# Kernel tuning notes

Hardware: AMD Instinct MI355X
Metric: run time of the kernel (lower is better)

## Reference

```python
import jax, jax.numpy as jnp
import numpy as np

B, Q, K, DQ, DK, H, DV = 4, 1024, 1024, 256, 256, 64, 256

def setup_inputs() -> dict:
    key = jax.random.key(0)
    k1, k2, k3, k4, k5, k6 = jax.random.split(key, 6)
    queries = jax.random.normal(k1, (B, Q, DQ), dtype=jnp.float32)
    keys = jax.random.normal(k2, (B, K, DK), dtype=jnp.float32)
    values = jax.random.normal(k3, (B, K, DV), dtype=jnp.float32)
    # learned params (stored as (in, out) so x @ W matches nn.Linear)
    W_q = jax.random.normal(k4, (DQ, H), dtype=jnp.float32) / np.sqrt(DQ)
    W_k = jax.random.normal(k5, (DK, H), dtype=jnp.float32) / np.sqrt(DK)
    w_v = jax.random.normal(k6, (H,), dtype=jnp.float32) / np.sqrt(H)
    return {"queries": queries, "keys": keys, "values": values,
            "W_q": W_q, "W_k": W_k, "w_v": w_v}

def reference(queries, keys, values, W_q, W_k, w_v):
    # projections: [B,Q,H], [B,K,H]
    q = jnp.einsum('bqd,dh->bqh', queries, W_q)
    k = jnp.einsum('bkd,dh->bkh', keys, W_k)
    # broadcast add -> tanh -> reduce with w_v: scores [B,Q,K]
    features = jnp.tanh(q[:, :, None, :] + k[:, None, :, :])  # [B,Q,K,H]
    scores = jnp.einsum('bqkh,h->bqk', features, w_v)
    attn = jax.nn.softmax(scores, axis=-1)  # dropout is identity in eval
    return jnp.einsum('bqk,bkv->bqv', attn, values)
```

## Files before the change

kernel.cpp:

```cpp
#include <hip/hip_runtime.h>

#define Bn 4
#define Qn 1024
#define Kn 1024
#define Dd 256
#define Hh 64
#define Dv 256
#define TQ 16

typedef __attribute__((ext_vector_type(8))) short short8;
typedef __attribute__((ext_vector_type(4))) float floatx4;
typedef __attribute__((ext_vector_type(2))) float floatx2;

__device__ __forceinline__ floatx2 fma2(floatx2 a, floatx2 b, floatx2 c) {
    return __builtin_elementwise_fma(a, b, c);
}
__device__ __forceinline__ floatx2 mk2(float x, float y) {
    floatx2 r; r.x = x; r.y = y; return r;
}

__device__ __forceinline__ short f32_to_bf16(float x) {
    unsigned u = __float_as_uint(x);
    unsigned r = u + 0x7fffu + ((u >> 16) & 1u);
    return (short)(r >> 16);
}
__device__ __forceinline__ float bf16_to_f32(short h) {
    return __uint_as_float(((unsigned)(unsigned short)h) << 16);
}

__global__ __launch_bounds__(256) void prep_kernel(const float* __restrict__ Xq,
                                                   const float* __restrict__ Wq,
                                                   const float* __restrict__ Xk,
                                                   const float* __restrict__ Wk,
                                                   const float* __restrict__ V,
                                                   float* __restrict__ Eq,
                                                   float* __restrict__ Ekt,
                                                   short* __restrict__ Vhi,
                                                   short* __restrict__ Vlo) {
    __shared__ float tile[32 * 261];
    int t = threadIdx.x;
    if (blockIdx.x < 256) {
        int gw = blockIdx.x * 4 + (t >> 6);
        int h = t & 63;
        int side = gw >> 9;
        int row0 = (gw & 511) * 8;
        const float* X = side ? Xk : Xq;
        const float* W = side ? Wk : Wq;
        float acc[8] = {0.f, 0.f, 0.f, 0.f, 0.f, 0.f, 0.f, 0.f};
        for (int d4 = 0; d4 < Dd / 4; ++d4) {
            float w0 = W[(d4 * 4 + 0) * Hh + h];
            float w1 = W[(d4 * 4 + 1) * Hh + h];
            float w2 = W[(d4 * 4 + 2) * Hh + h];
            float w3 = W[(d4 * 4 + 3) * Hh + h];
            #pragma unroll
            for (int r = 0; r < 8; ++r) {
                float4 xv = ((const float4*)(X + (size_t)(row0 + r) * Dd))[d4];
                acc[r] = fmaf(xv.x, w0, acc[r]);
                acc[r] = fmaf(xv.y, w1, acc[r]);
                acc[r] = fmaf(xv.z, w2, acc[r]);
                acc[r] = fmaf(xv.w, w3, acc[r]);
            }
        }
        #pragma unroll
        for (int r = 0; r < 8; ++r) {
            int row = row0 + r;
            float e = __expf(2.f * acc[r]);
            if (!side) {
                Eq[(size_t)row * Hh + h] = e;
            } else {
                int b = row >> 10, k = row & 1023;
                Ekt[((size_t)b * Hh + h) * Kn + k] = e;
            }
        }
    } else {
        int blk = blockIdx.x - 256;
        int b = blk >> 5;
        int kt = blk & 31;
        const float* Vg = V + (b * Kn + kt * 32) * Dv;
        for (int i = 0; i < 8; ++i) {
            int k = i * 4 + (t >> 6);
            int n4 = (t & 63) * 4;
            float4 v = *(const float4*)(Vg + k * Dv + n4);
            tile[k * 261 + n4 + 0] = v.x;
            tile[k * 261 + n4 + 1] = v.y;
            tile[k * 261 + n4 + 2] = v.z;
            tile[k * 261 + n4 + 3] = v.w;
        }
        __syncthreads();
        int wave = t >> 6, l = t & 63;
        int n_in = l & 15, kc = l >> 4;
        for (int p = 0; p < 4; ++p) {
            int nt = wave * 4 + p;
            int n = nt * 16 + n_in;
            short8 hi, lo;
            #pragma unroll
            for (int j = 0; j < 8; ++j) {
                float x = tile[(kc * 8 + j) * 261 + n];
                short hs = f32_to_bf16(x);
                hi[j] = hs;
                lo[j] = f32_to_bf16(x - bf16_to_f32(hs));
            }
            size_t base = (((size_t)(b * 32 + kt) * 16 + nt) * 512) + (size_t)l * 8;
            *(short8*)(Vhi + base) = hi;
            *(short8*)(Vlo + base) = lo;
        }
    }
}

__global__ __launch_bounds__(1024, 4) void attn_kernel(const float* __restrict__ Eq,
                                                       const float* __restrict__ Ekt,
                                                       const short* __restrict__ Vhi,
                                                       const short* __restrict__ Vlo,
                                                       const float* __restrict__ wv,
                                                       float* __restrict__ out) {
    __shared__ __align__(16) unsigned sc[TQ * 1028];
    __shared__ float wsum[16 * TQ];
    __shared__ float rinv_s[TQ];

    int tid = threadIdx.x;
    int blk = blockIdx.x;
    int b = (blk & 7) >> 1;
    int tile = (blk >> 3) * 2 + (blk & 1);
    int qbase = tile * TQ;

    const float* kb = Ekt + (size_t)b * Hh * Kn;
    const float* qp = Eq + (size_t)(b * Qn + qbase) * Hh;
    const float4* wv4 = (const float4*)wv;
    floatx2 s2[TQ / 2];
    #pragma unroll
    for (int i = 0; i < TQ / 2; ++i) { s2[i].x = 0.f; s2[i].y = 0.f; }

    float e0 = kb[0 * Kn + tid];
    float e1 = kb[1 * Kn + tid];
    float e2 = kb[2 * Kn + tid];
    float e3 = kb[3 * Kn + tid];
    floatx2 one2 = mk2(1.f, 1.f);
    for (int h4 = 0; h4 < Hh / 4; ++h4) {
        float n0, n1, n2, n3;
        if (h4 < Hh / 4 - 1) {
            const float* kn = kb + (h4 + 1) * 4 * Kn;
            n0 = kn[0 * Kn + tid];
            n1 = kn[1 * Kn + tid];
            n2 = kn[2 * Kn + tid];
            n3 = kn[3 * Kn + tid];
        }
        float4 w4 = wv4[h4];
        floatx2 e0s = mk2(e0, e0), e1s = mk2(e1, e1);
        floatx2 e2s = mk2(e2, e2), e3s = mk2(e3, e3);
        floatx2 wx = mk2(w4.x, w4.x), wy = mk2(w4.y, w4.y);
        floatx2 wz = mk2(w4.z, w4.z), ww = mk2(w4.w, w4.w);
        #pragma unroll
        for (int qq = 0; qq < TQ; qq += 2) {
            float4 qva = *(const float4*)(qp + qq * Hh + h4 * 4);
            float4 qvb = *(const float4*)(qp + (qq + 1) * Hh + h4 * 4);
            floatx2 A = fma2(mk2(qva.x, qvb.x), e0s, one2);
            floatx2 B = fma2(mk2(qva.y, qvb.y), e1s, one2);
            floatx2 C = fma2(mk2(qva.z, qvb.z), e2s, one2);
            floatx2 D = fma2(mk2(qva.w, qvb.w), e3s, one2);
            floatx2 AB = A * B;
            floatx2 CD = C * D;
            floatx2 ABCD = AB * CD;
            floatx2 NAB = fma2(wx, B, wy * A);
            floatx2 NCD = fma2(wz, D, ww * C);
            floatx2 NUM = fma2(NCD, AB, NAB * CD);
            floatx2 R = mk2(__builtin_amdgcn_rcpf(ABCD.x),
                            __builtin_amdgcn_rcpf(ABCD.y));
            s2[qq >> 1] = fma2(NUM, R, s2[qq >> 1]);
        }
        e0 = n0; e1 = n1; e2 = n2; e3 = n3;
    }

    unsigned short* sp = (unsigned short*)sc;
    float part[TQ];
    #pragma unroll
    for (int q = 0; q < TQ; ++q) {
        float sq = (q & 1) ? s2[q >> 1].y : s2[q >> 1].x;
        float p = __expf(-2.f * sq);
        part[q] = p;
        short hs = f32_to_bf16(p);
        sp[q * 2056 + tid] = (unsigned short)hs;
        sp[q * 2056 + 1024 + tid] = (unsigned short)f32_to_bf16(p - bf16_to_f32(hs));
    }

    int wave = tid >> 6, lane = tid & 63;
    #pragma unroll
    for (int q = 0; q < TQ; ++q) {
        #pragma unroll
        for (int off = 32; off >= 1; off >>= 1)
            part[q] += __shfl_xor(part[q], off, 64);
    }
    if (lane == 0) {
        #pragma unroll
        for (int q = 0; q < TQ; ++q) wsum[wave * TQ + q] = part[q];
    }
    __syncthreads();

    {
        float v = (lane < 16) ? wsum[lane * TQ + wave] : 0.f;
        v += __shfl_xor(v, 8, 64);
        v += __shfl_xor(v, 4, 64);
        v += __shfl_xor(v, 2, 64);
        v += __shfl_xor(v, 1, 64);
        if (lane == 0) rinv_s[wave] = 1.f / v;
    }
    __syncthreads();

    int qf = lane & 15, kc = lane >> 4;
    floatx4 acc = {0.f, 0.f, 0.f, 0.f};
    const char* scb = (const char*)sc;
    for (int kt = 0; kt < 32; ++kt) {
        short8 bhi = *(const short8*)(scb + qf * 4112 + kt * 64 + kc * 16);
        short8 blo = *(const short8*)(scb + qf * 4112 + 2048 + kt * 64 + kc * 16);
        size_t base = (((size_t)(b * 32 + kt) * 16 + wave) * 512) + (size_t)lane * 8;
        short8 ah = *(const short8*)(Vhi + base);
        short8 al = *(const short8*)(Vlo + base);
        acc = __builtin_amdgcn_mfma_f32_16x16x32_bf16(ah, bhi, acc, 0, 0, 0);
        acc = __builtin_amdgcn_mfma_f32_16x16x32_bf16(al, bhi, acc, 0, 0, 0);
        acc = __builtin_amdgcn_mfma_f32_16x16x32_bf16(ah, blo, acc, 0, 0, 0);
    }
    {
        float r = rinv_s[qf];
        float* ob = out + ((size_t)(b * Qn + qbase + qf)) * Dv + wave * 16 + kc * 4;
        float4 o = { acc[0] * r, acc[1] * r, acc[2] * r, acc[3] * r };
        *(float4*)ob = o;
    }
}

extern "C" void kernel_launch(void* const* d_in, const int* in_sizes, int n_in,
                              void* d_out, int out_size, void* d_ws, size_t ws_size,
                              hipStream_t stream) {
    const float* queries = (const float*)d_in[0];
    const float* keys    = (const float*)d_in[1];
    const float* values  = (const float*)d_in[2];
    const float* W_q     = (const float*)d_in[3];
    const float* W_k     = (const float*)d_in[4];
    const float* w_v     = (const float*)d_in[5];
    float* out = (float*)d_out;

    float* Eq  = (float*)d_ws;
    float* Ekt = Eq + Bn * Qn * Hh;
    short* Vhi = (short*)(Ekt + Bn * Kn * Hh);
    short* Vlo = Vhi + (size_t)Bn * Kn * Dv;

    prep_kernel<<<384, 256, 0, stream>>>(queries, W_q, keys, W_k, values,
                                         Eq, Ekt, Vhi, Vlo);
    attn_kernel<<<Bn * (Qn / TQ), 1024, 0, stream>>>(Eq, Ekt, Vhi, Vlo, w_v, out);
}
```

Before: 126.0 us.

## Compute Q/K projections with split-bf16 MFMA instead of scalar FMA

The projection part of the prep kernel now splits W and X into bf16 hi/lo pairs and runs three bf16 MFMA passes per tile to approximate fp32 accuracy. W is staged in LDS in MFMA fragment order, and each wave handles 16 rows. The projection now uses 128 blocks instead of 256 scalar-FMA blocks, which cuts the prep grid from 384 to 256. The risks are the conversion overhead, fewer blocks in flight, and a small accuracy loss because the lo*lo term is dropped.

New measurement: 115.3 us. -8.5%, faster.

```diff
diff --git a/kernel.cpp b/kernel.cpp
--- a/kernel.cpp
+++ b/kernel.cpp
@@ -37,43 +37,82 @@
                                                    float* __restrict__ Ekt,
                                                    short* __restrict__ Vhi,
                                                    short* __restrict__ Vlo) {
-    __shared__ float tile[32 * 261];
+    __shared__ __align__(16) char smem[65536];
     int t = threadIdx.x;
-    if (blockIdx.x < 256) {
-        int gw = blockIdx.x * 4 + (t >> 6);
-        int h = t & 63;
-        int side = gw >> 9;
-        int row0 = (gw & 511) * 8;
+    if (blockIdx.x < 128) {
+        short* wh_lds = (short*)smem;
+        short* wl_lds = (short*)(smem + 32768);
+        int side = blockIdx.x >> 6;
         const float* X = side ? Xk : Xq;
         const float* W = side ? Wk : Wq;
-        float acc[8] = {0.f, 0.f, 0.f, 0.f, 0.f, 0.f, 0.f, 0.f};
-        for (int d4 = 0; d4 < Dd / 4; ++d4) {
-            float w0 = W[(d4 * 4 + 0) * Hh + h];
-            float w1 = W[(d4 * 4 + 1) * Hh + h];
-            float w2 = W[(d4 * 4 + 2) * Hh + h];
-            float w3 = W[(d4 * 4 + 3) * Hh + h];
-            #pragma unroll
-            for (int r = 0; r < 8; ++r) {
-                float4 xv = ((const float4*)(X + (size_t)(row0 + r) * Dd))[d4];
-                acc[r] = fmaf(xv.x, w0, acc[r]);
-                acc[r] = fmaf(xv.y, w1, acc[r]);
-                acc[r] = fmaf(xv.z, w2, acc[r]);
-                acc[r] = fmaf(xv.w, w3, acc[r]);
-            }
-        }
-        #pragma unroll
-        for (int r = 0; r < 8; ++r) {
-            int row = row0 + r;
-            float e = __expf(2.f * acc[r]);
-            if (!side) {
-                Eq[(size_t)row * Hh + h] = e;
-            } else {
-                int b = row >> 10, k = row & 1023;
-                Ekt[((size_t)b * Hh + h) * Kn + k] = e;
+        #pragma unroll
+        for (int si = 0; si < 8; ++si) {
+            int s = t * 8 + si;
+            int l = s & 63, ct = (s >> 6) & 3, kt = s >> 8;
+            int col = ct * 16 + (l & 15);
+            int kb = kt * 32 + (l >> 4) * 8;
+            short8 hi, lo;
+            #pragma unroll
+            for (int j = 0; j < 8; ++j) {
+                float x = W[(kb + j) * Hh + col];
+                short hs = f32_to_bf16(x);
+                hi[j] = hs;
+                lo[j] = f32_to_bf16(x - bf16_to_f32(hs));
+            }
+            *(short8*)(wh_lds + s * 8) = hi;
+            *(short8*)(wl_lds + s * 8) = lo;
+        }
+        __syncthreads();
+        int wave = t >> 6, l = t & 63;
+        int r0 = ((blockIdx.x & 63) * 4 + wave) * 16;
+        const float* xrow = X + (size_t)(r0 + (l & 15)) * Dd + (l >> 4) * 8;
+        short8 ah[8], al[8];
+        #pragma unroll
+        for (int kt = 0; kt < 8; ++kt) {
+            floatx4 a = *(const floatx4*)(xrow + kt * 32);
+            floatx4 b = *(const floatx4*)(xrow + kt * 32 + 4);
+            #pragma unroll
+            for (int j = 0; j < 4; ++j) {
+                short hs = f32_to_bf16(a[j]);
+                ah[kt][j] = hs;
+                al[kt][j] = f32_to_bf16(a[j] - bf16_to_f32(hs));
+                short hs2 = f32_to_bf16(b[j]);
+                ah[kt][j + 4] = hs2;
+                al[kt][j + 4] = f32_to_bf16(b[j] - bf16_to_f32(hs2));
+            }
+        }
+        floatx4 acc[4];
+        #pragma unroll
+        for (int ct = 0; ct < 4; ++ct) acc[ct] = (floatx4){0.f, 0.f, 0.f, 0.f};
+        #pragma unroll
+        for (int kt = 0; kt < 8; ++kt) {
+            #pragma unroll
+            for (int ct = 0; ct < 4; ++ct) {
+                short8 wh = *(const short8*)(wh_lds + ((kt * 4 + ct) * 64 + l) * 8);
+                short8 wl = *(const short8*)(wl_lds + ((kt * 4 + ct) * 64 + l) * 8);
+                acc[ct] = __builtin_amdgcn_mfma_f32_16x16x32_bf16(ah[kt], wh, acc[ct], 0, 0, 0);
+                acc[ct] = __builtin_amdgcn_mfma_f32_16x16x32_bf16(al[kt], wh, acc[ct], 0, 0, 0);
+                acc[ct] = __builtin_amdgcn_mfma_f32_16x16x32_bf16(ah[kt], wl, acc[ct], 0, 0, 0);
+            }
+        }
+        #pragma unroll
+        for (int ct = 0; ct < 4; ++ct) {
+            #pragma unroll
+            for (int i = 0; i < 4; ++i) {
+                float e = __expf(2.f * acc[ct][i]);
+                int row = r0 + (l >> 4) * 4 + i;
+                int h = ct * 16 + (l & 15);
+                if (!side) {
+                    Eq[(size_t)row * Hh + h] = e;
+                } else {
+                    int b = row >> 10, k = row & 1023;
+                    Ekt[((size_t)b * Hh + h) * Kn + k] = e;
+                }
             }
         }
     } else {
-        int blk = blockIdx.x - 256;
+        float* tile = (float*)smem;
+        int blk = blockIdx.x - 128;
         int b = blk >> 5;
         int kt = blk & 31;
         const float* Vg = V + (b * Kn + kt * 32) * Dv;
@@ -242,7 +281,7 @@
     short* Vhi = (short*)(Ekt + Bn * Kn * Hh);
     short* Vlo = Vhi + (size_t)Bn * Kn * Dv;
 
-    prep_kernel<<<384, 256, 0, stream>>>(queries, W_q, keys, W_k, values,
+    prep_kernel<<<256, 256, 0, stream>>>(queries, W_q, keys, W_k, values,
                                          Eq, Ekt, Vhi, Vlo);
     attn_kernel<<<Bn * (Qn / TQ), 1024, 0, stream>>>(Eq, Ekt, Vhi, Vlo, w_v, out);
 }
```
